# Kernel optimization log

Hardware: AMD Instinct MI355X
Metric: run time of the kernel (lower is better)

The kernel has to match this reference:

```python
import jax, jax.numpy as jnp
import numpy as np

HEADS = 8
MEM_LEN = 32


def _mha(q, k, v, Wq, bq, Wk, bk, Wv, bv, Wo, bo):
    # torch nn.MultiheadAttention, batch_first=False. q: [Lq,B,E], k/v: [Lk,B,E]
    Lq, B, E = q.shape
    d = E // HEADS

    def proj(t, W, b):
        p = t @ W.T + b
        return p.reshape(t.shape[0], B, HEADS, d).transpose(1, 2, 0, 3)  # [B,h,L,d]

    qh, kh, vh = proj(q, Wq, bq), proj(k, Wk, bk), proj(v, Wv, bv)
    scale = 1.0 / jnp.sqrt(jnp.asarray(d, q.dtype))
    att = jax.nn.softmax(jnp.einsum('bhqd,bhkd->bhqk', qh * scale, kh), axis=-1)
    out = jnp.einsum('bhqk,bhkd->bhqd', att, vh)          # [B,h,Lq,d]
    out = out.transpose(2, 0, 1, 3).reshape(Lq, B, E)
    return out @ Wo.T + bo


def _forward(x, h, c, memK, memV, externalK, externalV,
             W_ih, W_hh, b_ih, b_hh,
             sWq, sbq, sWk, sbk, sWv, sbv, sWo, sbo,
             cWq, cbq, cWk, cbk, cWv, cbv, cWo, cbo,
             Wres, bres, Wrout, brout, Wcomp, bcomp, Wexp, bexp, Wgate, bgate):
    H = h.shape[1]
    # LSTMCell (torch gate order i, f, g, o)
    gates = x @ W_ih.T + b_ih + h @ W_hh.T + b_hh
    i, f, g, o = jnp.split(gates, 4, axis=1)
    c_next = jax.nn.sigmoid(f) * c + jax.nn.sigmoid(i) * jnp.tanh(g)
    h_lstm = jax.nn.sigmoid(o) * jnp.tanh(c_next)
    # append detached h_lstm to short memory, keep last MEM_LEN entries
    cur = jax.lax.stop_gradient(h_lstm)[None]                      # [1,B,H]
    memK_new = jnp.concatenate([memK, cur], axis=0)[-MEM_LEN:]     # [ML,B,H]
    memV_new = jnp.concatenate([memV, cur], axis=0)[-MEM_LEN:]
    qSelf = h_lstm[None]                                           # [1,B,H]
    self_out = _mha(qSelf, memK_new, memV_new, sWq, sbq, sWk, sbk, sWv, sbv, sWo, sbo)[0]
    ext_out = _mha(qSelf, externalK, externalV, cWq, cbq, cWk, cbk, cWv, cbv, cWo, cbo)[0]
    rw = jax.nn.softmax(h_lstm @ Wrout.T + brout, axis=1)          # [B,2] router
    routed_attn = rw[:, :1] * self_out + rw[:, 1:2] * ext_out
    routed = h_lstm + routed_attn + routed_attn @ Wres.T + bres
    temporal_summary = memK_new.mean(axis=0)                       # [B,H]
    compressed = temporal_summary @ Wcomp.T + bcomp                # [B,H//4]
    expanded = compressed @ Wexp.T + bexp                          # [B,H]
    reps = -(-H // compressed.shape[1])
    compressed_expanded = jnp.tile(compressed, (1, reps))[:, :H]
    gate = jax.nn.sigmoid(jnp.concatenate([x, routed], axis=1) @ Wgate.T + bgate)
    hCT = compressed_expanded + gate * (expanded - compressed_expanded)  # torch.lerp
    hFinal = (h_lstm + routed + hCT) / 3.0                         # dropout = identity (eval)
    return hFinal, h_lstm, c_next


def setup_inputs() -> dict:
    key = jax.random.key(0)
    ks = jax.random.split(key, 34)
    B, I, H, ML, EL = 2048, 1024, 1024, 32, 32
    BN = H // 4
    rn = lambda k, s, sc=1.0: jax.random.normal(k, s, dtype=jnp.float32) * sc
    return {
        'x': rn(ks[0], (B, I)), 'h': rn(ks[1], (B, H)), 'c': rn(ks[2], (B, H)),
        'memK': rn(ks[3], (ML, B, H)), 'memV': rn(ks[4], (ML, B, H)),
        'externalK': rn(ks[5], (EL, B, H)), 'externalV': rn(ks[6], (EL, B, H)),
        'W_ih': rn(ks[7], (4 * H, I), 0.02), 'W_hh': rn(ks[8], (4 * H, H), 0.02),
        'b_ih': jnp.zeros((4 * H,), jnp.float32), 'b_hh': jnp.zeros((4 * H,), jnp.float32),
        'sWq': rn(ks[9], (H, H), 0.02), 'sbq': rn(ks[10], (H,), 0.02),
        'sWk': rn(ks[11], (H, H), 0.02), 'sbk': rn(ks[12], (H,), 0.02),
        'sWv': rn(ks[13], (H, H), 0.02), 'sbv': rn(ks[14], (H,), 0.02),
        'sWo': rn(ks[15], (H, H), 0.02), 'sbo': rn(ks[16], (H,), 0.02),
        'cWq': rn(ks[17], (H, H), 0.02), 'cbq': rn(ks[18], (H,), 0.02),
        'cWk': rn(ks[19], (H, H), 0.02), 'cbk': rn(ks[20], (H,), 0.02),
        'cWv': rn(ks[21], (H, H), 0.02), 'cbv': rn(ks[22], (H,), 0.02),
        'cWo': rn(ks[23], (H, H), 0.02), 'cbo': rn(ks[24], (H,), 0.02),
        'Wres': rn(ks[25], (H, H), 0.02), 'bres': rn(ks[26], (H,), 0.02),
        'Wrout': rn(ks[27], (2, H), 0.02), 'brout': rn(ks[28], (2,), 0.02),
        'Wcomp': rn(ks[29], (BN, H), 0.02), 'bcomp': rn(ks[30], (BN,), 0.02),
        'Wexp': rn(ks[31], (H, BN), 0.02), 'bexp': rn(ks[32], (H,), 0.02),
        'Wgate': rn(ks[33], (H, I + H), 0.02), 'bgate': jnp.zeros((H,), jnp.float32),
    }


def reference(x, h, c, memK, memV, externalK, externalV,
              W_ih, W_hh, b_ih, b_hh,
              sWq, sbq, sWk, sbk, sWv, sbv, sWo, sbo,
              cWq, cbq, cWk, cbk, cWv, cbv, cWo, cbo,
              Wres, bres, Wrout, brout, Wcomp, bcomp, Wexp, bexp, Wgate, bgate):
    return _forward(x, h, c, memK, memV, externalK, externalV,
                    W_ih, W_hh, b_ih, b_hh,
                    sWq, sbq, sWk, sbk, sWv, sbv, sWo, sbo,
                    cWq, cbq, cWk, cbk, cWv, cbv, cWo, cbo,
                    Wres, bres, Wrout, brout, Wcomp, bcomp, Wexp, bexp, Wgate, bgate)
```

## Files before the change

kernel.cpp:

```cpp
#include <hip/hip_runtime.h>
#include <math.h>

typedef __attribute__((ext_vector_type(4))) float f32x4;
typedef __attribute__((ext_vector_type(8))) short bf16x8;
typedef __attribute__((ext_vector_type(4))) unsigned short u16x4;
typedef __attribute__((ext_vector_type(8))) unsigned short u16x8;

__device__ __forceinline__ unsigned short f2bf(float f) {
  unsigned u = __builtin_bit_cast(unsigned, f);
  u += 0x7fffu + ((u >> 16) & 1u);
  return (unsigned short)(u >> 16);
}
__device__ __forceinline__ float bf2f(unsigned short s) {
  return __builtin_bit_cast(float, (unsigned)s << 16);
}
__device__ __forceinline__ float sigmoidf_(float x) { return 1.f / (1.f + __expf(-x)); }

template <int TN, int ACAT, int BCAT, int EPI, int ABF16, int OBF16>
__global__ __launch_bounds__(256) void gemm_k(
    const void* __restrict__ A1, const void* __restrict__ A1b, int lda1, long aZ,
    const void* __restrict__ A2, int lda2, int Ksplit,
    const float* __restrict__ B1, const float* __restrict__ B1b, int ldb1, long bZ,
    const float* __restrict__ B2, int ldb2,
    const float* __restrict__ bias1, const float* __restrict__ bias1b, long biasZ,
    const float* __restrict__ bias2,
    void* __restrict__ C, void* __restrict__ Cb, int ldc, long cZ,
    int K, int zs, float scale,
    const float* __restrict__ P0, const float* __restrict__ P1,
    const float* __restrict__ P2, const float* __restrict__ P3) {
  constexpr int NBI = TN / 32;
  __shared__ unsigned short As[2][128][32];
  __shared__ unsigned short Bs[2][TN][32];
  const int t = threadIdx.x;
  const int lane = t & 63;
  const int wave = t >> 6;
  const int wr = wave >> 1, wc = wave & 1;

  const unsigned gx = gridDim.x, gy = gridDim.y;
  unsigned L = blockIdx.x + gx * (blockIdx.y + gy * blockIdx.z);
  const unsigned nwg = gx * gy * gridDim.z;
  L = (L & 7u) * (nwg >> 3) + (L >> 3);
  const int bn = L % gx;
  const unsigned r1 = L / gx;
  const int bm = r1 % gy;
  const int z = r1 / gy;

  const bool hi = z >= zs;
  const int zz = hi ? z - zs : z;
  const char* Abase = (const char*)(hi ? A1b : A1) + (long)zz * aZ * (ABF16 ? 2 : 4);
  const float* Bbase = (hi ? B1b : B1) + (long)zz * bZ;
  const float* biasp = hi ? bias1b : bias1;
  char* Czc = (char*)(hi ? Cb : C) + (long)zz * cZ * (OBF16 ? 2 : 4);

  const int ar = t >> 3;
  const int bc = (t & 7) * 4;

  const int kIters = K >> 5;
  u16x4 Ra[4], Rb[NBI];

  auto loadT = [&](int kt) {
    const int k0 = kt << 5;
    const char* Ap; int ldA, kA;
    if (ACAT == 1 && k0 >= Ksplit) { Ap = (const char*)A2; ldA = lda2; kA = k0 - Ksplit; }
    else { Ap = Abase; ldA = lda1; kA = k0; }
    const float* Bp; int ldB, kB;
    if (BCAT == 1 && k0 >= Ksplit) { Bp = B2; ldB = ldb2; kB = k0 - Ksplit; }
    else { Bp = Bbase; ldB = ldb1; kB = k0; }
#pragma unroll
    for (int i = 0; i < 4; ++i) {
      const long aoff = ((long)bm * 128 + ar + 32 * i) * ldA + kA + bc;
      if (ABF16) {
        Ra[i] = *(const u16x4*)((const unsigned short*)Ap + aoff);
      } else {
        f32x4 v = *(const f32x4*)((const float*)Ap + aoff);
        u16x4 pk;
        pk[0] = f2bf(v[0]); pk[1] = f2bf(v[1]); pk[2] = f2bf(v[2]); pk[3] = f2bf(v[3]);
        Ra[i] = pk;
      }
    }
#pragma unroll
    for (int i = 0; i < NBI; ++i) {
      f32x4 bv = *(const f32x4*)(Bp + ((long)bn * TN + ar + 32 * i) * ldB + kB + bc);
      u16x4 bp;
      bp[0] = f2bf(bv[0]); bp[1] = f2bf(bv[1]); bp[2] = f2bf(bv[2]); bp[3] = f2bf(bv[3]);
      Rb[i] = bp;
    }
  };

  loadT(0);

  f32x4 acc[4][NBI] = {};
  int p = 0;
  for (int kt = 0; kt < kIters; ++kt) {
    __syncthreads();
#pragma unroll
    for (int i = 0; i < 4; ++i) *(u16x4*)&As[p][ar + 32 * i][bc] = Ra[i];
#pragma unroll
    for (int i = 0; i < NBI; ++i) *(u16x4*)&Bs[p][ar + 32 * i][bc] = Rb[i];
    if (kt + 1 < kIters) loadT(kt + 1);
    __syncthreads();

    bf16x8 af[4], bfr[NBI];
#pragma unroll
    for (int mi = 0; mi < 4; ++mi)
      af[mi] = *(const bf16x8*)&As[p][wr * 64 + mi * 16 + (lane & 15)][(lane >> 4) * 8];
#pragma unroll
    for (int ni = 0; ni < NBI; ++ni)
      bfr[ni] = *(const bf16x8*)&Bs[p][wc * (TN / 2) + ni * 16 + (lane & 15)][(lane >> 4) * 8];
#pragma unroll
    for (int mi = 0; mi < 4; ++mi)
#pragma unroll
      for (int ni = 0; ni < NBI; ++ni)
        acc[mi][ni] = __builtin_amdgcn_mfma_f32_16x16x32_bf16(af[mi], bfr[ni], acc[mi][ni], 0, 0, 0);
    p ^= 1;
  }

  const int colb = bn * TN + wc * (TN / 2);
  const int rowb = bm * 128 + wr * 64;
#pragma unroll
  for (int mi = 0; mi < 4; ++mi) {
#pragma unroll
    for (int ni = 0; ni < NBI; ++ni) {
      f32x4 v = acc[mi][ni];
      const int col = colb + ni * 16 + (lane & 15);
      const int row0 = rowb + mi * 16 + ((lane >> 4) << 2);
      float bsum = 0.f;
      if (biasp) bsum += biasp[zz * biasZ + col];
      if (bias2) bsum += bias2[col];
#pragma unroll
      for (int q = 0; q < 4; ++q) {
        const long row = row0 + q;
        const long off = row * ldc + col;
        const float val = v[q] + bsum;
        if (EPI == 0) {
          if (OBF16) ((unsigned short*)Czc)[off] = f2bf(val * scale);
          else       ((float*)Czc)[off] = val * scale;
        } else if (EPI == 1) {
          ((float*)Czc)[off] = val + P0[off] + P1[off];
        } else if (EPI == 2) {
          const float g = sigmoidf_(val);
          const float ce = P0[row * 256 + (col & 255)];
          const float ex = P1[off];
          ((float*)Czc)[off] = (P2[off] + P3[off] + ce + g * (ex - ce)) * (1.f / 3.f);
        } else if (EPI == 3) {
          ((unsigned short*)Czc)[off] = f2bf(val * P0[2 * row + (hi ? 1 : 0)]);
        } else {
          ((float*)Czc)[off] = val + P2[2 * row] * P0[col] + P2[2 * row + 1] * P1[col];
        }
      }
    }
  }
}

__global__ __launch_bounds__(256) void transpose_k(const float* __restrict__ in0,
                                                   float* __restrict__ out0,
                                                   const float* __restrict__ in1,
                                                   float* __restrict__ out1, int n) {
  __shared__ float tile[64][65];
  const float* in = blockIdx.z ? in1 : in0;
  float* out = blockIdx.z ? out1 : out0;
  const int tr = blockIdx.y, tc = blockIdx.x, t = threadIdx.x;
#pragma unroll
  for (int it = 0; it < 16; ++it) {
    int idx = t + 256 * it;
    int r = idx >> 6, c = idx & 63;
    tile[r][c] = in[(long)(tr * 64 + r) * n + tc * 64 + c];
  }
  __syncthreads();
#pragma unroll
  for (int it = 0; it < 16; ++it) {
    int idx = t + 256 * it;
    int rr = idx >> 6, cc = idx & 63;
    out[(long)(tc * 64 + rr) * n + tr * 64 + cc] = tile[cc][rr];
  }
}

__global__ __launch_bounds__(256) void lstm_k(const float* __restrict__ gates,
                                              const float* __restrict__ c_in,
                                              const float* __restrict__ Wr,
                                              const float* __restrict__ br,
                                              float* __restrict__ c_out,
                                              float* __restrict__ h_ws,
                                              float* __restrict__ h_out,
                                              float* __restrict__ rw) {
  const int b = blockIdx.x, t = threadIdx.x;
  const long base = (long)b * 1024 + t * 4;
  const float* gb = gates + (long)b * 4096 + t * 4;
  f32x4 gi = *(const f32x4*)(gb);
  f32x4 gf = *(const f32x4*)(gb + 1024);
  f32x4 gg = *(const f32x4*)(gb + 2048);
  f32x4 go = *(const f32x4*)(gb + 3072);
  f32x4 cv = *(const f32x4*)(c_in + base);
  f32x4 cn, hv;
#pragma unroll
  for (int q = 0; q < 4; ++q) {
    float cc = sigmoidf_(gf[q]) * cv[q] + sigmoidf_(gi[q]) * tanhf(gg[q]);
    cn[q] = cc;
    hv[q] = sigmoidf_(go[q]) * tanhf(cc);
  }
  *(f32x4*)(c_out + base) = cn;
  *(f32x4*)(h_ws + base) = hv;
  *(f32x4*)(h_out + base) = hv;
  f32x4 w0 = *(const f32x4*)(Wr + t * 4);
  f32x4 w1 = *(const f32x4*)(Wr + 1024 + t * 4);
  float a0 = hv[0] * w0[0] + hv[1] * w0[1] + hv[2] * w0[2] + hv[3] * w0[3];
  float a1 = hv[0] * w1[0] + hv[1] * w1[1] + hv[2] * w1[2] + hv[3] * w1[3];
#pragma unroll
  for (int m = 32; m >= 1; m >>= 1) {
    a0 += __shfl_xor(a0, m);
    a1 += __shfl_xor(a1, m);
  }
  __shared__ float red[8];
  if ((t & 63) == 0) { red[t >> 6] = a0; red[4 + (t >> 6)] = a1; }
  __syncthreads();
  if (t == 0) {
    float z0 = red[0] + red[1] + red[2] + red[3] + br[0];
    float z1 = red[4] + red[5] + red[6] + red[7] + br[1];
    float mx = fmaxf(z0, z1);
    float e0 = __expf(z0 - mx), e1 = __expf(z1 - mx);
    float s = e0 + e1;
    rw[2 * b] = e0 / s;
    rw[2 * b + 1] = e1 / s;
  }
}

__global__ __launch_bounds__(256) void scores9_k(
    const float* __restrict__ memK, const float* __restrict__ extK,
    const float* __restrict__ hl,
    const unsigned short* __restrict__ qtS, const unsigned short* __restrict__ qtE,
    float* __restrict__ P_g, float* __restrict__ ts) {
  const int NB = 2048, H = 1024;
  __shared__ float qtf[256 * 36];
  __shared__ float S_lds[32][8];
  unsigned flat = blockIdx.x + gridDim.x * blockIdx.y;
  flat = (flat & 7u) * 512u + (flat >> 3);
  const int b = flat & 2047;
  const bool self = (flat >> 11) == 0;
  const int t = threadIdx.x;

  {
    const unsigned short* qtb = (self ? qtS : qtE) + (long)b * 8192;
#pragma unroll
    for (int i = 0; i < 4; ++i) {
      const int chunk = t + 256 * i;
      const int hh = chunk >> 7;
      const int pos = (chunk & 127) * 8;
      u16x8 qv = *(const u16x8*)(qtb + hh * 1024 + pos);
      const int kq0 = pos >> 2;
      f32x4 a, bb;
      a[0] = bf2f(qv[0]); a[1] = bf2f(qv[1]); a[2] = bf2f(qv[2]); a[3] = bf2f(qv[3]);
      bb[0] = bf2f(qv[4]); bb[1] = bf2f(qv[5]); bb[2] = bf2f(qv[6]); bb[3] = bf2f(qv[7]);
      *(f32x4*)&qtf[kq0 * 36 + hh * 4] = a;
      *(f32x4*)&qtf[(kq0 + 1) * 36 + hh * 4] = bb;
    }
  }
  __syncthreads();

  const int r = t >> 3, sub = t & 7;
  const float* Kr = self ? ((r < 31) ? memK + ((long)(r + 1) * NB + b) * H : hl + (long)b * H)
                         : extK + ((long)r * NB + b) * H;
  float acc[8] = {};
#pragma unroll
  for (int i = 0; i < 32; i += 4) {
    f32x4 kv[4];
#pragma unroll
    for (int u = 0; u < 4; ++u) kv[u] = *(const f32x4*)(Kr + ((i + u) * 8 + sub) * 4);
#pragma unroll
    for (int u = 0; u < 4; ++u) {
      const float* qp = &qtf[((i + u) * 8 + sub) * 36];
#pragma unroll
      for (int hh = 0; hh < 8; ++hh) {
        f32x4 q = *(const f32x4*)(qp + hh * 4);
        acc[hh] += kv[u][0] * q[0] + kv[u][1] * q[1] + kv[u][2] * q[2] + kv[u][3] * q[3];
      }
    }
  }
#pragma unroll
  for (int hh = 0; hh < 8; ++hh) {
    acc[hh] += __shfl_xor(acc[hh], 1);
    acc[hh] += __shfl_xor(acc[hh], 2);
    acc[hh] += __shfl_xor(acc[hh], 4);
  }
  if (sub == 0) {
#pragma unroll
    for (int hh = 0; hh < 8; ++hh) S_lds[r][hh] = acc[hh];
  }
  __syncthreads();
  {
    const int l = t & 31, hh = t >> 5;
    float Sv = S_lds[l][hh];
    float mx = Sv;
#pragma unroll
    for (int m = 16; m >= 1; m >>= 1) mx = fmaxf(mx, __shfl_xor(mx, m, 32));
    float pr = __expf(Sv - mx);
    float su = pr;
#pragma unroll
    for (int m = 16; m >= 1; m >>= 1) su += __shfl_xor(su, m, 32);
    P_g[((long)b * 2 + (self ? 0 : 1)) * 256 + l * 8 + hh] = pr / su;
  }
  if (self) {
    const float* Kb = memK + (long)b * H + 4 * t;
    f32x4 a = {};
#pragma unroll
    for (int l = 0; l < 31; ++l) a += *(const f32x4*)(Kb + (long)(l + 1) * NB * H);
    a += *(const f32x4*)(hl + (long)b * H + 4 * t);
    *(f32x4*)(ts + (long)b * H + 4 * t) = a * (1.f / 32.f);
  }
}

__global__ __launch_bounds__(256) void mix8_k(
    const float* __restrict__ memV, const float* __restrict__ extV,
    const float* __restrict__ hl,
    const float* __restrict__ P_g,
    unsigned short* __restrict__ mixS, unsigned short* __restrict__ mixE) {
  const int NB = 2048, H = 1024;
  __shared__ float P_lds[256];
  unsigned flat = blockIdx.x + gridDim.x * blockIdx.y;
  flat = (flat & 7u) * 512u + (flat >> 3);
  const int b = flat & 2047;
  const bool self = (flat >> 11) == 0;
  const int t = threadIdx.x;

  P_lds[t] = P_g[((long)b * 2 + (self ? 0 : 1)) * 256 + t];
  __syncthreads();

  const float* Vbase = (self ? memV + (long)NB * H : extV) + (long)b * H + 4 * t;
  const float* hlp = hl + (long)b * H + 4 * t;
  f32x4 acc[8] = {};
#pragma unroll
  for (int l = 0; l < 32; l += 2) {
    f32x4 vv0 = *(const f32x4*)(Vbase + (long)l * NB * H);
    f32x4 vv1 = *(const f32x4*)((self && l + 1 == 31) ? hlp
                                                      : Vbase + (long)(l + 1) * NB * H);
    const float* Pl0 = &P_lds[l * 8];
    const float* Pl1 = &P_lds[(l + 1) * 8];
#pragma unroll
    for (int hh = 0; hh < 8; ++hh) acc[hh] += Pl0[hh] * vv0;
#pragma unroll
    for (int hh = 0; hh < 8; ++hh) acc[hh] += Pl1[hh] * vv1;
  }
  unsigned short* mixp = (self ? mixS : mixE) + (long)b * 8192;
#pragma unroll
  for (int hh = 0; hh < 8; ++hh) {
    u16x4 pk;
    pk[0] = f2bf(acc[hh][0]); pk[1] = f2bf(acc[hh][1]);
    pk[2] = f2bf(acc[hh][2]); pk[3] = f2bf(acc[hh][3]);
    *(u16x4*)(mixp + hh * 1024 + 4 * t) = pk;
  }
}

extern "C" void kernel_launch(void* const* d_in, const int* in_sizes, int n_in,
                              void* d_out, int out_size, void* d_ws, size_t ws_size,
                              hipStream_t stream) {
  const float* x    = (const float*)d_in[0];
  const float* h    = (const float*)d_in[1];
  const float* c    = (const float*)d_in[2];
  const float* memK = (const float*)d_in[3];
  const float* memV = (const float*)d_in[4];
  const float* extK = (const float*)d_in[5];
  const float* extV = (const float*)d_in[6];
  const float* W_ih = (const float*)d_in[7];
  const float* W_hh = (const float*)d_in[8];
  const float* b_ih = (const float*)d_in[9];
  const float* b_hh = (const float*)d_in[10];
  const float* sWq = (const float*)d_in[11];
  const float* sbq = (const float*)d_in[12];
  const float* sWk = (const float*)d_in[13];
  const float* sWv = (const float*)d_in[15];
  const float* sbv = (const float*)d_in[16];
  const float* sWo = (const float*)d_in[17];
  const float* sbo = (const float*)d_in[18];
  const float* cWq = (const float*)d_in[19];
  const float* cbq = (const float*)d_in[20];
  const float* cWk = (const float*)d_in[21];
  const float* cWv = (const float*)d_in[23];
  const float* cbv = (const float*)d_in[24];
  const float* cWo = (const float*)d_in[25];
  const float* cbo = (const float*)d_in[26];
  const float* Wres = (const float*)d_in[27];
  const float* bres = (const float*)d_in[28];
  const float* Wrout = (const float*)d_in[29];
  const float* brout = (const float*)d_in[30];
  const float* Wcomp = (const float*)d_in[31];
  const float* bcomp = (const float*)d_in[32];
  const float* Wexp = (const float*)d_in[33];
  const float* bexp = (const float*)d_in[34];
  const float* Wgate = (const float*)d_in[35];
  const float* bgate = (const float*)d_in[36];
  (void)in_sizes; (void)n_in; (void)out_size; (void)ws_size;

  float* out = (float*)d_out;
  float* w = (float*)d_ws;
  const long M1 = 1024 * 1024;
  float* gates   = w;
  float* P_g     = w;
  float* hl      = w + 8 * M1;
  unsigned short* qsS = (unsigned short*)(w + 10 * M1);
  unsigned short* qsE = (unsigned short*)(w + 12 * M1);
  float* wkTs    = w + 14 * M1;
  float* wkTc    = w + 15 * M1;
  unsigned short* qtS = (unsigned short*)(w + 16 * M1);
  unsigned short* qtE = (unsigned short*)(w + 32 * M1);
  unsigned short* mixS = (unsigned short*)(w + 48 * M1);
  unsigned short* mixE = (unsigned short*)(w + 64 * M1);
  float* ts      = w + 80 * M1;
  unsigned short* attnS = (unsigned short*)(w + 82 * M1);
  unsigned short* attnE = (unsigned short*)(w + 84 * M1);
  float* rw      = w + 90 * M1;
  float* rattn   = w + 91 * M1;
  float* routed  = w + 93 * M1;
  float* comp    = w + 95 * M1;
  float* expd    = w + 96 * M1;

  float* hFinal_out = out;
  float* hl_out     = out + 2 * M1;
  float* cn_out     = out + 4 * M1;

  const float scaleq = 0.08838834764831845f;
  const int ZBIG = 1 << 30;
  dim3 blk(256);
  const float* nf = nullptr;

  gemm_k<128, 1, 1, 0, 0, 0><<<dim3(32, 16, 1), blk, 0, stream>>>(
      x, nullptr, 1024, 0, h, 1024, 1024,
      W_ih, nf, 1024, 0, W_hh, 1024,
      b_ih, nf, 0, b_hh,
      gates, nullptr, 4096, 0,
      2048, ZBIG, 1.f, nf, nf, nf, nf);

  transpose_k<<<dim3(16, 16, 2), blk, 0, stream>>>(sWk, wkTs, cWk, wkTc, 1024);

  lstm_k<<<2048, blk, 0, stream>>>(gates, c, Wrout, brout, cn_out, hl, hl_out, rw);

  gemm_k<128, 0, 0, 0, 0, 1><<<dim3(8, 16, 2), blk, 0, stream>>>(
      hl, hl, 1024, 0, nullptr, 0, 0,
      sWq, cWq, 1024, 0, nf, 0,
      sbq, cbq, 0, nf,
      qsS, qsE, 1024, 0,
      1024, 1, scaleq, nf, nf, nf, nf);

  gemm_k<128, 0, 0, 0, 1, 1><<<dim3(8, 16, 16), blk, 0, stream>>>(
      qsS, qsE, 1024, 128, nullptr, 0, 0,
      wkTs, wkTc, 1024, 128, nf, 0,
      nf, nf, 0, nf,
      qtS, qtE, 8192, 1024,
      128, 8, 1.f, nf, nf, nf, nf);

  scores9_k<<<dim3(2048, 2), blk, 0, stream>>>(memK, extK, hl, qtS, qtE, P_g, ts);
  mix8_k<<<dim3(2048, 2), blk, 0, stream>>>(memV, extV, hl, P_g, mixS, mixE);

  gemm_k<64, 0, 0, 3, 1, 1><<<dim3(2, 16, 16), blk, 0, stream>>>(
      mixS, mixE, 8192, 1024, nullptr, 0, 0,
      sWv, cWv, 1024, 131072, nf, 0,
      sbv, cbv, 128, nf,
      attnS, attnE, 1024, 128,
      1024, 8, 1.f, rw, nf, nf, nf);

  gemm_k<64, 1, 1, 4, 1, 0><<<dim3(16, 16, 1), blk, 0, stream>>>(
      attnS, nullptr, 1024, 0, attnE, 1024, 1024,
      sWo, nf, 1024, 0, cWo, 1024,
      nf, nf, 0, nf,
      rattn, nullptr, 1024, 0,
      2048, ZBIG, 1.f, sbo, cbo, rw, nf);

  gemm_k<64, 0, 0, 1, 0, 0><<<dim3(16, 16, 1), blk, 0, stream>>>(
      rattn, nullptr, 1024, 0, nullptr, 0, 0,
      Wres, nf, 1024, 0, nf, 0,
      bres, nf, 0, nf,
      routed, nullptr, 1024, 0,
      1024, ZBIG, 1.f, hl, rattn, nf, nf);

  gemm_k<64, 0, 0, 0, 0, 0><<<dim3(4, 16, 1), blk, 0, stream>>>(
      ts, nullptr, 1024, 0, nullptr, 0, 0,
      Wcomp, nf, 1024, 0, nf, 0,
      bcomp, nf, 0, nf,
      comp, nullptr, 256, 0,
      1024, ZBIG, 1.f, nf, nf, nf, nf);
  gemm_k<64, 0, 0, 0, 0, 0><<<dim3(16, 16, 1), blk, 0, stream>>>(
      comp, nullptr, 256, 0, nullptr, 0, 0,
      Wexp, nf, 256, 0, nf, 0,
      bexp, nf, 0, nf,
      expd, nullptr, 1024, 0,
      256, ZBIG, 1.f, nf, nf, nf, nf);

  gemm_k<64, 1, 0, 2, 0, 0><<<dim3(16, 16, 1), blk, 0, stream>>>(
      x, nullptr, 1024, 0, routed, 1024, 1024,
      Wgate, nf, 2048, 0, nf, 0,
      bgate, nf, 0, nf,
      hFinal_out, nullptr, 1024, 0,
      2048, ZBIG, 1.f, comp, expd, hl, routed);
}
```

Before: 788.5 us.

## Pre-convert weights and activations to bf16 once before GEMMs

Adds a batched conversion kernel that turns all fp32 weights and the x/h inputs into bf16 buffers up front. The transpose kernel now writes bf16, and the LSTM and residual epilogues also emit bf16 copies. GEMMs gain a BBF16 path so they load bf16 operands directly instead of converting fp32 to bf16 in their load loops. This halves the bytes the GEMMs read, at the cost of an extra conversion pass that reads all fp32 weights every call and writes their bf16 copies.

```diff
diff --git a/kernel.cpp b/kernel.cpp
--- a/kernel.cpp
+++ b/kernel.cpp
@@ -16,12 +16,28 @@
 }
 __device__ __forceinline__ float sigmoidf_(float x) { return 1.f / (1.f + __expf(-x)); }
 
-template <int TN, int ACAT, int BCAT, int EPI, int ABF16, int OBF16>
+struct CJob { const float* s; unsigned short* d; int nblk; };
+struct CJobs { CJob j[14]; };
+
+__global__ __launch_bounds__(256) void conv_k(CJobs jb) {
+  int b = blockIdx.x;
+  int i = 0;
+  while (b >= jb.j[i].nblk) { b -= jb.j[i].nblk; ++i; }
+  const long base = (long)b * 2048 + threadIdx.x * 8;
+  f32x4 a = *(const f32x4*)(jb.j[i].s + base);
+  f32x4 c = *(const f32x4*)(jb.j[i].s + base + 4);
+  u16x8 o;
+  o[0] = f2bf(a[0]); o[1] = f2bf(a[1]); o[2] = f2bf(a[2]); o[3] = f2bf(a[3]);
+  o[4] = f2bf(c[0]); o[5] = f2bf(c[1]); o[6] = f2bf(c[2]); o[7] = f2bf(c[3]);
+  *(u16x8*)(jb.j[i].d + base) = o;
+}
+
+template <int TN, int ACAT, int BCAT, int EPI, int ABF16, int BBF16, int OBF16>
 __global__ __launch_bounds__(256) void gemm_k(
     const void* __restrict__ A1, const void* __restrict__ A1b, int lda1, long aZ,
     const void* __restrict__ A2, int lda2, int Ksplit,
-    const float* __restrict__ B1, const float* __restrict__ B1b, int ldb1, long bZ,
-    const float* __restrict__ B2, int ldb2,
+    const void* __restrict__ B1, const void* __restrict__ B1b, int ldb1, long bZ,
+    const void* __restrict__ B2, int ldb2,
     const float* __restrict__ bias1, const float* __restrict__ bias1b, long biasZ,
     const float* __restrict__ bias2,
     void* __restrict__ C, void* __restrict__ Cb, int ldc, long cZ,
@@ -48,7 +64,7 @@
   const bool hi = z >= zs;
   const int zz = hi ? z - zs : z;
   const char* Abase = (const char*)(hi ? A1b : A1) + (long)zz * aZ * (ABF16 ? 2 : 4);
-  const float* Bbase = (hi ? B1b : B1) + (long)zz * bZ;
+  const char* Bbase = (const char*)(hi ? B1b : B1) + (long)zz * bZ * (BBF16 ? 2 : 4);
   const float* biasp = hi ? bias1b : bias1;
   char* Czc = (char*)(hi ? Cb : C) + (long)zz * cZ * (OBF16 ? 2 : 4);
 
@@ -63,8 +79,8 @@
     const char* Ap; int ldA, kA;
     if (ACAT == 1 && k0 >= Ksplit) { Ap = (const char*)A2; ldA = lda2; kA = k0 - Ksplit; }
     else { Ap = Abase; ldA = lda1; kA = k0; }
-    const float* Bp; int ldB, kB;
-    if (BCAT == 1 && k0 >= Ksplit) { Bp = B2; ldB = ldb2; kB = k0 - Ksplit; }
+    const char* Bp; int ldB, kB;
+    if (BCAT == 1 && k0 >= Ksplit) { Bp = (const char*)B2; ldB = ldb2; kB = k0 - Ksplit; }
     else { Bp = Bbase; ldB = ldb1; kB = k0; }
 #pragma unroll
     for (int i = 0; i < 4; ++i) {
@@ -80,10 +96,15 @@
     }
 #pragma unroll
     for (int i = 0; i < NBI; ++i) {
-      f32x4 bv = *(const f32x4*)(Bp + ((long)bn * TN + ar + 32 * i) * ldB + kB + bc);
-      u16x4 bp;
-      bp[0] = f2bf(bv[0]); bp[1] = f2bf(bv[1]); bp[2] = f2bf(bv[2]); bp[3] = f2bf(bv[3]);
-      Rb[i] = bp;
+      const long boff = ((long)bn * TN + ar + 32 * i) * ldB + kB + bc;
+      if (BBF16) {
+        Rb[i] = *(const u16x4*)((const unsigned short*)Bp + boff);
+      } else {
+        f32x4 bv = *(const f32x4*)((const float*)Bp + boff);
+        u16x4 bp;
+        bp[0] = f2bf(bv[0]); bp[1] = f2bf(bv[1]); bp[2] = f2bf(bv[2]); bp[3] = f2bf(bv[3]);
+        Rb[i] = bp;
+      }
     }
   };
 
@@ -136,7 +157,9 @@
           if (OBF16) ((unsigned short*)Czc)[off] = f2bf(val * scale);
           else       ((float*)Czc)[off] = val * scale;
         } else if (EPI == 1) {
-          ((float*)Czc)[off] = val + P0[off] + P1[off];
+          const float r2 = val + P0[off] + P1[off];
+          ((float*)Czc)[off] = r2;
+          if (Cb) ((unsigned short*)Cb)[off] = f2bf(r2);
         } else if (EPI == 2) {
           const float g = sigmoidf_(val);
           const float ce = P0[row * 256 + (col & 255)];
@@ -153,12 +176,12 @@
 }
 
 __global__ __launch_bounds__(256) void transpose_k(const float* __restrict__ in0,
-                                                   float* __restrict__ out0,
+                                                   unsigned short* __restrict__ out0,
                                                    const float* __restrict__ in1,
-                                                   float* __restrict__ out1, int n) {
+                                                   unsigned short* __restrict__ out1, int n) {
   __shared__ float tile[64][65];
   const float* in = blockIdx.z ? in1 : in0;
-  float* out = blockIdx.z ? out1 : out0;
+  unsigned short* out = blockIdx.z ? out1 : out0;
   const int tr = blockIdx.y, tc = blockIdx.x, t = threadIdx.x;
 #pragma unroll
   for (int it = 0; it < 16; ++it) {
@@ -171,7 +194,7 @@
   for (int it = 0; it < 16; ++it) {
     int idx = t + 256 * it;
     int rr = idx >> 6, cc = idx & 63;
-    out[(long)(tc * 64 + rr) * n + tr * 64 + cc] = tile[cc][rr];
+    out[(long)(tc * 64 + rr) * n + tr * 64 + cc] = f2bf(tile[cc][rr]);
   }
 }
 
@@ -182,6 +205,7 @@
                                               float* __restrict__ c_out,
                                               float* __restrict__ h_ws,
                                               float* __restrict__ h_out,
+                                              unsigned short* __restrict__ hlb,
                                               float* __restrict__ rw) {
   const int b = blockIdx.x, t = threadIdx.x;
   const long base = (long)b * 1024 + t * 4;
@@ -201,6 +225,9 @@
   *(f32x4*)(c_out + base) = cn;
   *(f32x4*)(h_ws + base) = hv;
   *(f32x4*)(h_out + base) = hv;
+  u16x4 hp;
+  hp[0] = f2bf(hv[0]); hp[1] = f2bf(hv[1]); hp[2] = f2bf(hv[2]); hp[3] = f2bf(hv[3]);
+  *(u16x4*)(hlb + base) = hp;
   f32x4 w0 = *(const f32x4*)(Wr + t * 4);
   f32x4 w1 = *(const f32x4*)(Wr + 1024 + t * 4);
   float a0 = hv[0] * w0[0] + hv[1] * w0[1] + hv[2] * w0[2] + hv[3] * w0[3];
@@ -392,13 +419,14 @@
   float* out = (float*)d_out;
   float* w = (float*)d_ws;
   const long M1 = 1024 * 1024;
+  const long U = 1024 * 1024;
+  unsigned short* ub = (unsigned short*)w;
+
   float* gates   = w;
   float* P_g     = w;
   float* hl      = w + 8 * M1;
   unsigned short* qsS = (unsigned short*)(w + 10 * M1);
   unsigned short* qsE = (unsigned short*)(w + 12 * M1);
-  float* wkTs    = w + 14 * M1;
-  float* wkTc    = w + 15 * M1;
   unsigned short* qtS = (unsigned short*)(w + 16 * M1);
   unsigned short* qtE = (unsigned short*)(w + 32 * M1);
   unsigned short* mixS = (unsigned short*)(w + 48 * M1);
@@ -412,6 +440,25 @@
   float* comp    = w + 95 * M1;
   float* expd    = w + 96 * M1;
 
+  unsigned short* Wihb  = ub + 48 * U;
+  unsigned short* Whhb  = ub + 52 * U;
+  unsigned short* xb    = ub + 56 * U;
+  unsigned short* hb    = ub + 58 * U;
+  unsigned short* sWqb  = ub + 60 * U;
+  unsigned short* cWqb  = ub + 61 * U;
+  unsigned short* sWvb  = ub + 62 * U;
+  unsigned short* cWvb  = ub + 63 * U;
+  unsigned short* sWob  = ub + 80 * U;
+  unsigned short* cWob  = ub + 81 * U;
+  unsigned short* Wresb = ub + 82 * U;
+  unsigned short* Wcompb= ub + 83 * U;
+  unsigned short* Wexpb = ub + 84 * U;
+  unsigned short* Wgateb= ub + 85 * U;
+  unsigned short* wkTsb = ub + 87 * U;
+  unsigned short* wkTcb = ub + 88 * U;
+  unsigned short* hlb   = ub + 89 * U;
+  unsigned short* routedb = ub + 91 * U;
+
   float* hFinal_out = out;
   float* hl_out     = out + 2 * M1;
   float* cn_out     = out + 4 * M1;
@@ -420,28 +467,46 @@
   const int ZBIG = 1 << 30;
   dim3 blk(256);
   const float* nf = nullptr;
-
-  gemm_k<128, 1, 1, 0, 0, 0><<<dim3(32, 16, 1), blk, 0, stream>>>(
-      x, nullptr, 1024, 0, h, 1024, 1024,
-      W_ih, nf, 1024, 0, W_hh, 1024,
+  const void* nv = nullptr;
+
+  CJobs jb;
+  jb.j[0] = {x, xb, 1024};
+  jb.j[1] = {h, hb, 1024};
+  jb.j[2] = {W_ih, Wihb, 2048};
+  jb.j[3] = {W_hh, Whhb, 2048};
+  jb.j[4] = {sWq, sWqb, 512};
+  jb.j[5] = {cWq, cWqb, 512};
+  jb.j[6] = {sWv, sWvb, 512};
+  jb.j[7] = {cWv, cWvb, 512};
+  jb.j[8] = {sWo, sWob, 512};
+  jb.j[9] = {cWo, cWob, 512};
+  jb.j[10] = {Wres, Wresb, 512};
+  jb.j[11] = {Wcomp, Wcompb, 128};
+  jb.j[12] = {Wexp, Wexpb, 128};
+  jb.j[13] = {Wgate, Wgateb, 1024};
+  conv_k<<<11008, blk, 0, stream>>>(jb);
+
+  transpose_k<<<dim3(16, 16, 2), blk, 0, stream>>>(sWk, wkTsb, cWk, wkTcb, 1024);
+
+  gemm_k<128, 1, 1, 0, 1, 1, 0><<<dim3(32, 16, 1), blk, 0, stream>>>(
+      xb, nv, 1024, 0, hb, 1024, 1024,
+      Wihb, nv, 1024, 0, Whhb, 1024,
       b_ih, nf, 0, b_hh,
       gates, nullptr, 4096, 0,
       2048, ZBIG, 1.f, nf, nf, nf, nf);
 
-  transpose_k<<<dim3(16, 16, 2), blk, 0, stream>>>(sWk, wkTs, cWk, wkTc, 1024);
-
-  lstm_k<<<2048, blk, 0, stream>>>(gates, c, Wrout, brout, cn_out, hl, hl_out, rw);
-
-  gemm_k<128, 0, 0, 0, 0, 1><<<dim3(8, 16, 2), blk, 0, stream>>>(
-      hl, hl, 1024, 0, nullptr, 0, 0,
-      sWq, cWq, 1024, 0, nf, 0,
+  lstm_k<<<2048, blk, 0, stream>>>(gates, c, Wrout, brout, cn_out, hl, hl_out, hlb, rw);
+
+  gemm_k<128, 0, 0, 0, 1, 1, 1><<<dim3(8, 16, 2), blk, 0, stream>>>(
+      hlb, hlb, 1024, 0, nv, 0, 0,
+      sWqb, cWqb, 1024, 0, nv, 0,
       sbq, cbq, 0, nf,
       qsS, qsE, 1024, 0,
       1024, 1, scaleq, nf, nf, nf, nf);
 
-  gemm_k<128, 0, 0, 0, 1, 1><<<dim3(8, 16, 16), blk, 0, stream>>>(
-      qsS, qsE, 1024, 128, nullptr, 0, 0,
-      wkTs, wkTc, 1024, 128, nf, 0,
+  gemm_k<128, 0, 0, 0, 1, 1, 1><<<dim3(8, 16, 16), blk, 0, stream>>>(
+      qsS, qsE, 1024, 128, nv, 0, 0,
+      wkTsb, wkTcb, 1024, 128, nv, 0,
       nf, nf, 0, nf,
       qtS, qtE, 8192, 1024,
       128, 8, 1.f, nf, nf, nf, nf);
@@ -449,43 +514,43 @@
   scores9_k<<<dim3(2048, 2), blk, 0, stream>>>(memK, extK, hl, qtS, qtE, P_g, ts);
   mix8_k<<<dim3(2048, 2), blk, 0, stream>>>(memV, extV, hl, P_g, mixS, mixE);
 
-  gemm_k<64, 0, 0, 3, 1, 1><<<dim3(2, 16, 16), blk, 0, stream>>>(
-      mixS, mixE, 8192, 1024, nullptr, 0, 0,
-      sWv, cWv, 1024, 131072, nf, 0,
+  gemm_k<64, 0, 0, 3, 1, 1, 1><<<dim3(2, 16, 16), blk, 0, stream>>>(
+      mixS, mixE, 8192, 1024, nv, 0, 0,
+      sWvb, cWvb, 1024, 131072, nv, 0,
       sbv, cbv, 128, nf,
       attnS, attnE, 1024, 128,
       1024, 8, 1.f, rw, nf, nf, nf);
 
-  gemm_k<64, 1, 1, 4, 1, 0><<<dim3(16, 16, 1), blk, 0, stream>>>(
-      attnS, nullptr, 1024, 0, attnE, 1024, 1024,
-      sWo, nf, 1024, 0, cWo, 1024,
+  gemm_k<64, 1, 1, 4, 1, 1, 0><<<dim3(16, 16, 1), blk, 0, stream>>>(
+      attnS, nv, 1024, 0, attnE, 1024, 1024,
+      sWob, nv, 1024, 0, cWob, 1024,
       nf, nf, 0, nf,
       rattn, nullptr, 1024, 0,
       2048, ZBIG, 1.f, sbo, cbo, rw, nf);
 
-  gemm_k<64, 0, 0, 1, 0, 0><<<dim3(16, 16, 1), blk, 0, stream>>>(
-      rattn, nullptr, 1024, 0, nullptr, 0, 0,
-      Wres, nf, 1024, 0, nf, 0,
+  gemm_k<64, 0, 0, 1, 0, 1, 0><<<dim3(16, 16, 1), blk, 0, stream>>>(
+      rattn, nv, 1024, 0, nv, 0, 0,
+      Wresb, nv, 1024, 0, nv, 0,
       bres, nf, 0, nf,
-      routed, nullptr, 1024, 0,
+      routed, routedb, 1024, 0,
       1024, ZBIG, 1.f, hl, rattn, nf, nf);
 
-  gemm_k<64, 0, 0, 0, 0, 0><<<dim3(4, 16, 1), blk, 0, stream>>>(
-      ts, nullptr, 1024, 0, nullptr, 0, 0,
-      Wcomp, nf, 1024, 0, nf, 0,
+  gemm_k<64, 0, 0, 0, 0, 1, 0><<<dim3(4, 16, 1), blk, 0, stream>>>(
+      ts, nv, 1024, 0, nv, 0, 0,
+      Wcompb, nv, 1024, 0, nv, 0,
       bcomp, nf, 0, nf,
       comp, nullptr, 256, 0,
       1024, ZBIG, 1.f, nf, nf, nf, nf);
-  gemm_k<64, 0, 0, 0, 0, 0><<<dim3(16, 16, 1), blk, 0, stream>>>(
-      comp, nullptr, 256, 0, nullptr, 0, 0,
-      Wexp, nf, 256, 0, nf, 0,
+  gemm_k<64, 0, 0, 0, 0, 1, 0><<<dim3(16, 16, 1), blk, 0, stream>>>(
+      comp, nv, 256, 0, nv, 0, 0,
+      Wexpb, nv, 256, 0, nv, 0,
       bexp, nf, 0, nf,
       expd, nullptr, 1024, 0,
       256, ZBIG, 1.f, nf, nf, nf, nf);
 
-  gemm_k<64, 1, 0, 2, 0, 0><<<dim3(16, 16, 1), blk, 0, stream>>>(
-      x, nullptr, 1024, 0, routed, 1024, 1024,
-      Wgate, nf, 2048, 0, nf, 0,
+  gemm_k<64, 1, 0, 2, 1, 1, 0><<<dim3(16, 16, 1), blk, 0, stream>>>(
+      xb, nv, 1024, 0, routedb, 1024, 1024,
+      Wgateb, nv, 2048, 0, nv, 0,
       bgate, nf, 0, nf,
       hFinal_out, nullptr, 1024, 0,
       2048, ZBIG, 1.f, comp, expd, hl, routed);
```

New measurement: 660.8 us. 16.2% less time.
